# Kernel tuning notes

Hardware: AMD Instinct MI355X
Metric: run time of the kernel (lower is better)

The kernel has to match this reference:

```python
import jax, jax.numpy as jnp
import numpy as np

D_MODEL = 1024
N_HEADS = 16
D_HEAD = D_MODEL // N_HEADS
ROPE_BASE = 10000.0
EPS = float(jnp.finfo(jnp.float32).eps)  # torch RMSNorm default eps


def _rmsnorm(x, g):
    # x: (..., d_head), g: (d_head,)
    var = jnp.mean(x * x, axis=-1, keepdims=True)
    return x * jax.lax.rsqrt(var + EPS) * g


def _rope(x, pos):
    # x: (B, H, L, d), pos: (L,) int
    d = x.shape[-1]
    inv_freq = 1.0 / (ROPE_BASE ** (jnp.arange(0, d, 2, dtype=jnp.float32) / d))  # (d/2,)
    ang = pos.astype(jnp.float32)[:, None] * inv_freq[None, :]                    # (L, d/2)
    cos, sin = jnp.cos(ang), jnp.sin(ang)                                         # (L, d/2)
    x1, x2 = jnp.split(x, 2, axis=-1)
    return jnp.concatenate([x1 * cos - x2 * sin, x1 * sin + x2 * cos], axis=-1)


def setup_inputs() -> dict:
    key = jax.random.key(0)
    ks = jax.random.split(key, 6)
    B, Lq, Lk = 4, 2048, 2048
    s = 0.02
    return {
        "queries": jax.random.normal(ks[0], (B, Lq, D_MODEL), dtype=jnp.float32),
        "kv": jax.random.normal(ks[1], (B, Lk, D_MODEL), dtype=jnp.float32),
        "Wq": jax.random.normal(ks[2], (D_MODEL, D_MODEL), dtype=jnp.float32) * s,
        "Wkv": jax.random.normal(ks[3], (D_MODEL, 2 * D_MODEL), dtype=jnp.float32) * s,
        "Wout": jax.random.normal(ks[4], (D_MODEL, D_MODEL), dtype=jnp.float32) * s,
        "g_q": jnp.ones((D_HEAD,), dtype=jnp.float32),
        "g_k": jnp.ones((D_HEAD,), dtype=jnp.float32),
        "pos_q": jnp.arange(Lq, dtype=jnp.int64 if jax.config.jax_enable_x64 else jnp.int32),
        "pos_k": jnp.arange(Lk, dtype=jnp.int64 if jax.config.jax_enable_x64 else jnp.int32),
    }


def reference(queries, kv, Wq, Wkv, Wout, g_q, g_k, pos_q, pos_k):
    B, Lq, D = queries.shape
    Lk = kv.shape[1]
    H, d = N_HEADS, D_HEAD
    # projections (bias=False)
    q = (queries @ Wq).reshape(B, Lq, H, d).transpose(0, 2, 1, 3)          # (B,H,Lq,d)
    kvp = (kv @ Wkv).reshape(B, Lk, H, 2 * d).transpose(0, 2, 1, 3)        # (B,H,Lk,2d)
    k, v = kvp[..., :d], kvp[..., d:]
    # per-head RMSNorm on q/k
    q = _rmsnorm(q, g_q)
    k = _rmsnorm(k, g_k)
    # RoPE
    q = _rope(q, pos_q)
    k = _rope(k, pos_k)
    # attention (non-causal, no mask, no dropout)
    scale = d ** -0.5
    scores = jnp.einsum("bhqd,bhkd->bhqk", q, k) * scale                   # (B,H,Lq,Lk)
    attn = jax.nn.softmax(scores, axis=-1)
    y = jnp.einsum("bhqk,bhkd->bhqd", attn, v)                             # (B,H,Lq,d)
    y = y.transpose(0, 2, 1, 3).reshape(B, Lq, D)
    return y @ Wout
```

## Files before the change

kernel.cpp:

```cpp
#include <hip/hip_runtime.h>

#define DEVI __device__ __forceinline__

typedef __bf16 bf16;
typedef __attribute__((ext_vector_type(8))) __bf16 bf16x8v;
typedef __attribute__((ext_vector_type(4))) __bf16 bf16x4v;
typedef __attribute__((ext_vector_type(16))) float f32x16;

constexpr int LKV = 2048;

DEVI void gload16(const void* g, void* l) {
  __builtin_amdgcn_global_load_lds((__attribute__((address_space(1))) void*)g,
                                   (__attribute__((address_space(3))) void*)l, 16, 0, 0);
}

DEVI bf16x8v ldfrag(const bf16* base, int row, int clog) {
  int cphys = clog ^ (row & 7);
  return *(const bf16x8v*)(base + row * 64 + cphys * 8);
}

DEVI unsigned pk2(float a, float b) {
  unsigned short ha = __builtin_bit_cast(unsigned short, (__bf16)a);
  unsigned short hb = __builtin_bit_cast(unsigned short, (__bf16)b);
  return (unsigned)ha | ((unsigned)hb << 16);
}

__global__ void cast_bf16_kernel(const float* __restrict__ in, bf16* __restrict__ out, int n8) {
  int i = blockIdx.x * blockDim.x + threadIdx.x;
  if (i >= n8) return;
  long base = (long)i * 8;
  float4 a = *(const float4*)(in + base);
  float4 b = *(const float4*)(in + base + 4);
  bf16x8v v;
  v[0] = (bf16)a.x; v[1] = (bf16)a.y; v[2] = (bf16)a.z; v[3] = (bf16)a.w;
  v[4] = (bf16)b.x; v[5] = (bf16)b.y; v[6] = (bf16)b.z; v[7] = (bf16)b.w;
  *(bf16x8v*)(out + base) = v;
}

__global__ void wtrans_kernel(const float* __restrict__ W, bf16* __restrict__ Wt, int K, int N) {
  __shared__ float t[32][33];
  int n0 = blockIdx.x * 32, k0 = blockIdx.y * 32;
  int tx = threadIdx.x, ty = threadIdx.y;
  #pragma unroll
  for (int i = 0; i < 4; ++i) t[ty + i * 8][tx] = W[(long)(k0 + ty + i * 8) * N + n0 + tx];
  __syncthreads();
  #pragma unroll
  for (int i = 0; i < 4; ++i) Wt[(long)(n0 + ty + i * 8) * K + k0 + tx] = (bf16)t[tx][ty + i * 8];
}

template<bool OUT_BF16>
__global__ __launch_bounds__(256, 2)
void gemm_bf16_kernel(const bf16* __restrict__ A, const bf16* __restrict__ Bt,
                      void* __restrict__ C, int M, int N, int K, int NXB) {
  __shared__ bf16 As[128 * 64];
  __shared__ bf16 Bs[128 * 64];
  const int tid = threadIdx.x;
  const int wid = tid >> 6, lane = tid & 63;
  const int ln31 = lane & 31, hi = lane >> 5;
  const int wr = wid >> 1, wc = wid & 1;
  const int cpx = gridDim.x >> 3;
  const int wg = blockIdx.x;
  const int flat = (wg & 7) * cpx + (wg >> 3);
  const int by = flat / NXB, bx = flat - by * NXB;
  const int tM = by * 128, tN = bx * 128;
  f32x16 acc[2][2] = {};
  for (int kt = 0; kt < K; kt += 64) {
    #pragma unroll
    for (int p = 0; p < 8; ++p) {
      int cidx = p * 4 + wid;
      int row = (cidx & 15) * 8 + (lane >> 3);
      int clog = (lane & 7) ^ (row & 7);
      if (cidx < 16)
        gload16(A + (long)(tM + row) * K + kt + clog * 8, As + cidx * 512);
      else
        gload16(Bt + (long)(tN + row) * K + kt + clog * 8, Bs + (cidx - 16) * 512);
    }
    __syncthreads();
    #pragma unroll
    for (int st = 0; st < 4; ++st) {
      int clog = st * 2 + hi;
      bf16x8v a0 = ldfrag(As, wr * 64 + ln31, clog);
      bf16x8v a1 = ldfrag(As, wr * 64 + 32 + ln31, clog);
      bf16x8v b0 = ldfrag(Bs, wc * 64 + ln31, clog);
      bf16x8v b1 = ldfrag(Bs, wc * 64 + 32 + ln31, clog);
      acc[0][0] = __builtin_amdgcn_mfma_f32_32x32x16_bf16(a0, b0, acc[0][0], 0, 0, 0);
      acc[0][1] = __builtin_amdgcn_mfma_f32_32x32x16_bf16(a0, b1, acc[0][1], 0, 0, 0);
      acc[1][0] = __builtin_amdgcn_mfma_f32_32x32x16_bf16(a1, b0, acc[1][0], 0, 0, 0);
      acc[1][1] = __builtin_amdgcn_mfma_f32_32x32x16_bf16(a1, b1, acc[1][1], 0, 0, 0);
    }
    __syncthreads();
  }
  #pragma unroll
  for (int mi = 0; mi < 2; ++mi)
    #pragma unroll
    for (int ni = 0; ni < 2; ++ni)
      #pragma unroll
      for (int rr = 0; rr < 4; ++rr)
        #pragma unroll
        for (int j = 0; j < 4; ++j) {
          int mrow = tM + wr * 64 + mi * 32 + rr * 8 + hi * 4 + j;
          int ncol = tN + wc * 64 + ni * 32 + ln31;
          float v = acc[mi][ni][rr * 4 + j];
          if (OUT_BF16) ((bf16*)C)[(long)mrow * N + ncol] = (bf16)v;
          else          ((float*)C)[(long)mrow * N + ncol] = v;
        }
}

__global__ void rope_tab_kernel(const int* __restrict__ pos, float2* __restrict__ tab, float scale) {
  int idx = blockIdx.x * 256 + threadIdx.x;
  int l = idx >> 5, i = idx & 31;
  float ang = (float)pos[l] * __expf((float)i * -0.28782313662425575f);
  float sn, cs;
  sincosf(ang, &sn, &cs);
  tab[idx] = make_float2(cs * scale, sn * scale);
}

__global__ void rope_qk_kernel(const bf16* __restrict__ X, bf16* __restrict__ Out,
                               const float* __restrict__ g, const float2* __restrict__ tab,
                               int colStride, int colOff) {
  int tid = threadIdx.x; int wid = tid >> 6; int lane = tid & 63;
  long w = (long)blockIdx.x * 4 + wid;
  int h = (int)(w & 15); long bl = w >> 4;
  int l = (int)(bl & 2047); int b = (int)(bl >> 11);
  float x = (float)X[bl * colStride + h * colOff + lane];
  float ss = x * x;
  #pragma unroll
  for (int m = 32; m >= 1; m >>= 1) ss += __shfl_xor(ss, m);
  float rs = rsqrtf(ss * (1.0f / 64.0f) + 1.1920928955078125e-07f);
  x *= rs * g[lane];
  float other = __shfl_xor(x, 32);
  float2 cssn = tab[l * 32 + (lane & 31)];
  float y = x * cssn.x + ((lane < 32) ? -other : other) * cssn.y;
  int bh = b * 16 + h;
  Out[((long)bh * 2048 + l) * 64 + lane] = (bf16)y;
}

__global__ void transpose_v_kernel(const unsigned short* __restrict__ KVp, unsigned short* __restrict__ Vt) {
  __shared__ unsigned short t[64][65];
  int bh = blockIdx.y; int b = bh >> 4, h = bh & 15;
  long lt = (long)blockIdx.x * 64;
  int tid = threadIdx.x; int c = tid & 63; int r0 = tid >> 6;
  #pragma unroll
  for (int i = 0; i < 16; ++i) {
    int l = i * 4 + r0;
    t[l][c] = KVp[((long)(b * 2048) + lt + l) * 2048 + h * 128 + 64 + c];
  }
  __syncthreads();
  #pragma unroll
  for (int i = 0; i < 16; ++i) {
    int dv = i * 4 + r0;
    Vt[((long)(bh * 64 + dv)) * 2048 + lt + c] = t[c][dv];
  }
}

__global__ __launch_bounds__(256, 2)
void attn_kernel(const bf16* __restrict__ Q, const bf16* __restrict__ Kr,
                 const bf16* __restrict__ Vt, bf16* __restrict__ Y) {
  __shared__ bf16 Ks[2 * 4096];
  __shared__ bf16 Vs[2 * 4096];
  const int tid = threadIdx.x, wid = tid >> 6, lane = tid & 63;
  const int ln31 = lane & 31, hi = lane >> 5;
  const int wg = blockIdx.x;
  const int flat = (wg & 7) * 128 + (wg >> 3);
  const int bh = flat >> 4, qb = flat & 15;
  const int qg = qb * 128 + wid * 32 + ln31;

  const int rsub = lane >> 3, csub = lane & 7;
  int r0 = wid * 8 + rsub;        int s0 = csub ^ (r0 & 7);
  int r1 = (wid + 4) * 8 + rsub;  int s1 = csub ^ (r1 & 7);
  const bf16* gp0 = Kr + ((long)bh * 2048 + r0) * 64 + s0 * 8;
  const bf16* gp1 = Kr + ((long)bh * 2048 + r1) * 64 + s1 * 8;
  const bf16* gp2 = Vt + ((long)(bh * 64 + r0)) * 2048 + s0 * 8;
  const bf16* gp3 = Vt + ((long)(bh * 64 + r1)) * 2048 + s1 * 8;
  bf16* lk0 = Ks + wid * 512;
  bf16* lk1 = Ks + (wid + 4) * 512;
  bf16* lv0 = Vs + wid * 512;
  bf16* lv1 = Vs + (wid + 4) * 512;

  const bf16* Qrow = Q + ((long)bh * 2048 + qg) * 64;
  bf16x8v qf[4];
  #pragma unroll
  for (int st = 0; st < 4; ++st) qf[st] = *(const bf16x8v*)(Qrow + st * 16 + hi * 8);
  f32x16 o[2] = {};
  float srun = 0.0f;

  gload16(gp0, lk0); gp0 += 4096;
  gload16(gp1, lk1); gp1 += 4096;
  gload16(gp2, lv0); gp2 += 64;
  gload16(gp3, lv1); gp3 += 64;
  __syncthreads();

  int boff = 0;
  for (int kt = 0; kt < LKV; kt += 64) {
    if (kt + 64 < LKV) {
      int nb = boff ^ 4096;
      gload16(gp0, lk0 + nb); gp0 += 4096;
      gload16(gp1, lk1 + nb); gp1 += 4096;
      gload16(gp2, lv0 + nb); gp2 += 64;
      gload16(gp3, lv1 + nb); gp3 += 64;
    }
    const bf16* kb = Ks + boff;
    const bf16* vb = Vs + boff;

    f32x16 sT[2] = {};
    #pragma unroll
    for (int st = 0; st < 4; ++st) {
      int clog = st * 2 + hi;
      bf16x8v k0 = ldfrag(kb, ln31, clog);
      bf16x8v k1 = ldfrag(kb, 32 + ln31, clog);
      sT[0] = __builtin_amdgcn_mfma_f32_32x32x16_bf16(k0, qf[st], sT[0], 0, 0, 0);
      sT[1] = __builtin_amdgcn_mfma_f32_32x32x16_bf16(k1, qf[st], sT[1], 0, 0, 0);
    }

    float p0 = 0.0f, p1 = 0.0f, p2 = 0.0f, p3 = 0.0f;
    #pragma unroll
    for (int mf = 0; mf < 2; ++mf) {
      #pragma unroll
      for (int r = 0; r < 16; r += 4) {
        float e0 = __builtin_amdgcn_exp2f(sT[mf][r + 0]);
        float e1 = __builtin_amdgcn_exp2f(sT[mf][r + 1]);
        float e2 = __builtin_amdgcn_exp2f(sT[mf][r + 2]);
        float e3 = __builtin_amdgcn_exp2f(sT[mf][r + 3]);
        sT[mf][r + 0] = e0; sT[mf][r + 1] = e1; sT[mf][r + 2] = e2; sT[mf][r + 3] = e3;
        p0 += e0; p1 += e1; p2 += e2; p3 += e3;
      }
    }
    srun += (p0 + p1) + (p2 + p3);

    #pragma unroll
    for (int kb_ = 0; kb_ < 4; ++kb_) {
      int mf = kb_ >> 1; int rb = (kb_ & 1) * 8;
      unsigned w0 = pk2(sT[mf][rb + 0], sT[mf][rb + 1]);
      unsigned w1 = pk2(sT[mf][rb + 2], sT[mf][rb + 3]);
      unsigned w2 = pk2(sT[mf][rb + 4], sT[mf][rb + 5]);
      unsigned w3 = pk2(sT[mf][rb + 6], sT[mf][rb + 7]);
      asm("v_permlane32_swap_b32 %0, %1" : "+v"(w0), "+v"(w2));
      asm("v_permlane32_swap_b32 %0, %1" : "+v"(w1), "+v"(w3));
      uint4 uw = make_uint4(w0, w1, w2, w3);
      bf16x8v pf = __builtin_bit_cast(bf16x8v, uw);
      int clog = kb_ * 2 + hi;
      bf16x8v v0 = ldfrag(vb, ln31, clog);
      bf16x8v v1 = ldfrag(vb, 32 + ln31, clog);
      o[0] = __builtin_amdgcn_mfma_f32_32x32x16_bf16(v0, pf, o[0], 0, 0, 0);
      o[1] = __builtin_amdgcn_mfma_f32_32x32x16_bf16(v1, pf, o[1], 0, 0, 0);
    }
    __syncthreads();
    boff ^= 4096;
  }

  srun += __shfl_xor(srun, 32);
  float inv = 1.0f / srun;
  int b = bh >> 4, h = bh & 15;
  long orow = ((long)(b * 2048 + qg)) * 1024 + h * 64;
  #pragma unroll
  for (int mfo = 0; mfo < 2; ++mfo)
    #pragma unroll
    for (int rr = 0; rr < 4; ++rr) {
      bf16x4v wv;
      #pragma unroll
      for (int j = 0; j < 4; ++j) wv[j] = (bf16)(o[mfo][rr * 4 + j] * inv);
      *(bf16x4v*)(Y + orow + mfo * 32 + rr * 8 + hi * 4) = wv;
    }
}

extern "C" void kernel_launch(void* const* d_in, const int* in_sizes, int n_in,
                              void* d_out, int out_size, void* d_ws, size_t ws_size,
                              hipStream_t stream) {
  const float* queries = (const float*)d_in[0];
  const float* kv      = (const float*)d_in[1];
  const float* Wq      = (const float*)d_in[2];
  const float* Wkv     = (const float*)d_in[3];
  const float* Wout    = (const float*)d_in[4];
  const float* g_q     = (const float*)d_in[5];
  const float* g_k     = (const float*)d_in[6];
  const int*   pos_q   = (const int*)d_in[7];
  const int*   pos_k   = (const int*)d_in[8];

  char* ws = (char*)d_ws;
  bf16* Qb    = (bf16*)ws; ws += (long)8192 * 1024 * 2;
  bf16* KVb   = (bf16*)ws; ws += (long)8192 * 1024 * 2;
  bf16* Wqt   = (bf16*)ws; ws += (long)1024 * 1024 * 2;
  bf16* Wkvt  = (bf16*)ws; ws += (long)2048 * 1024 * 2;
  bf16* Woutt = (bf16*)ws; ws += (long)1024 * 1024 * 2;
  bf16* Qp    = (bf16*)ws; ws += (long)8192 * 1024 * 2;
  bf16* KVp   = (bf16*)ws; ws += (long)8192 * 2048 * 2;
  bf16* Qr    = (bf16*)ws; ws += (long)8192 * 1024 * 2;
  bf16* Kr    = (bf16*)ws; ws += (long)8192 * 1024 * 2;
  bf16* Vt    = (bf16*)ws; ws += (long)8192 * 1024 * 2;
  bf16* Y     = (bf16*)ws; ws += (long)8192 * 1024 * 2;
  float2* tabq = (float2*)ws; ws += (long)65536 * 8;
  float2* tabk = (float2*)ws; ws += (long)65536 * 8;

  rope_tab_kernel<<<256, 256, 0, stream>>>(pos_q, tabq, 0.18033688011112042f);
  rope_tab_kernel<<<256, 256, 0, stream>>>(pos_k, tabk, 1.0f);

  cast_bf16_kernel<<<4096, 256, 0, stream>>>(queries, Qb, 8192 * 1024 / 8);
  cast_bf16_kernel<<<4096, 256, 0, stream>>>(kv, KVb, 8192 * 1024 / 8);
  wtrans_kernel<<<dim3(32, 32), dim3(32, 8), 0, stream>>>(Wq, Wqt, 1024, 1024);
  wtrans_kernel<<<dim3(64, 32), dim3(32, 8), 0, stream>>>(Wkv, Wkvt, 1024, 2048);
  wtrans_kernel<<<dim3(32, 32), dim3(32, 8), 0, stream>>>(Wout, Woutt, 1024, 1024);

  gemm_bf16_kernel<true><<<512, 256, 0, stream>>>(Qb, Wqt, Qp, 8192, 1024, 1024, 8);
  gemm_bf16_kernel<true><<<1024, 256, 0, stream>>>(KVb, Wkvt, KVp, 8192, 2048, 1024, 16);

  rope_qk_kernel<<<32768, 256, 0, stream>>>(Qp, Qr, g_q, tabq, 1024, 64);
  rope_qk_kernel<<<32768, 256, 0, stream>>>(KVp, Kr, g_k, tabk, 2048, 128);
  transpose_v_kernel<<<dim3(32, 64), 256, 0, stream>>>((const unsigned short*)KVp, (unsigned short*)Vt);

  attn_kernel<<<1024, 256, 0, stream>>>(Qr, Kr, Vt, Y);

  gemm_bf16_kernel<false><<<512, 256, 0, stream>>>(Y, Woutt, d_out, 8192, 1024, 1024, 8);
}
```

Baseline: 367.2 us.

## Add 256x256-tile multi-stage GEMM for KV projection and raise MFMA priority

```diff
diff --git a/kernel.cpp b/kernel.cpp
--- a/kernel.cpp
+++ b/kernel.cpp
@@ -106,6 +106,85 @@
         }
 }
 
+DEVI void stage_region(const bf16* __restrict__ A, const bf16* __restrict__ Bt,
+                       long tM, long tN, int K, int s, bf16* Lds, int tid) {
+  bf16* region = Lds + ((((s >> 1) & 1) << 1) | (s & 1)) * 16384;
+  int kcol = (s >> 1) * 64 + (s & 1) * 32;
+  #pragma unroll
+  for (int q = 0; q < 4; ++q) {
+    int ci = q * 512 + tid;
+    int row = ci >> 3, phys = ci & 7;
+    int clog = phys ^ (row & 7);
+    const bf16* src = (clog < 4)
+      ? A  + (tM + row) * K + kcol + clog * 8
+      : Bt + (tN + row) * K + kcol + (clog - 4) * 8;
+    gload16(src, region + ci * 8);
+  }
+}
+
+__global__ __launch_bounds__(512, 2)
+void gemm256_kernel(const bf16* __restrict__ A, const bf16* __restrict__ Bt,
+                    bf16* __restrict__ C, int M, int N, int K, int NXB) {
+  __shared__ bf16 Lds[4 * 16384];
+  const int tid = threadIdx.x;
+  const int wid = tid >> 6, lane = tid & 63;
+  const int ln31 = lane & 31, hi = lane >> 5;
+  const int wm = wid >> 2, wn = wid & 3;
+  const int cpx = gridDim.x >> 3;
+  const int wg = blockIdx.x;
+  const int flat = (wg & 7) * cpx + (wg >> 3);
+  const int by = flat / NXB, bx = flat - by * NXB;
+  const long tM = (long)by * 256, tN = (long)bx * 256;
+  const int NS = (K >> 6) * 2;
+
+  f32x16 acc[4][2] = {};
+
+  stage_region(A, Bt, tM, tN, K, 0, Lds, tid);
+  stage_region(A, Bt, tM, tN, K, 1, Lds, tid);
+  stage_region(A, Bt, tM, tN, K, 2, Lds, tid);
+
+  for (int s = 0; s < NS; ++s) {
+    asm volatile("s_waitcnt vmcnt(8)" ::: "memory");
+    __builtin_amdgcn_s_barrier();
+    __builtin_amdgcn_sched_barrier(0);
+    stage_region(A, Bt, tM, tN, K, s + 3, Lds, tid);
+    const bf16* R = Lds + ((((s >> 1) & 1) << 1) | (s & 1)) * 16384;
+    bf16x8v a[4][2], b[2][2];
+    #pragma unroll
+    for (int mi = 0; mi < 4; ++mi)
+      #pragma unroll
+      for (int ks = 0; ks < 2; ++ks)
+        a[mi][ks] = ldfrag(R, wm * 128 + mi * 32 + ln31, ks * 2 + hi);
+    #pragma unroll
+    for (int ni = 0; ni < 2; ++ni)
+      #pragma unroll
+      for (int ks = 0; ks < 2; ++ks)
+        b[ni][ks] = ldfrag(R, wn * 64 + ni * 32 + ln31, 4 + ks * 2 + hi);
+    __builtin_amdgcn_s_setprio(1);
+    #pragma unroll
+    for (int ks = 0; ks < 2; ++ks)
+      #pragma unroll
+      for (int mi = 0; mi < 4; ++mi)
+        #pragma unroll
+        for (int ni = 0; ni < 2; ++ni)
+          acc[mi][ni] = __builtin_amdgcn_mfma_f32_32x32x16_bf16(a[mi][ks], b[ni][ks], acc[mi][ni], 0, 0, 0);
+    __builtin_amdgcn_s_setprio(0);
+  }
+
+  #pragma unroll
+  for (int mi = 0; mi < 4; ++mi)
+    #pragma unroll
+    for (int ni = 0; ni < 2; ++ni)
+      #pragma unroll
+      for (int rr = 0; rr < 4; ++rr)
+        #pragma unroll
+        for (int j = 0; j < 4; ++j) {
+          long mrow = tM + wm * 128 + mi * 32 + rr * 8 + hi * 4 + j;
+          long ncol = tN + wn * 64 + ni * 32 + ln31;
+          C[mrow * N + ncol] = (bf16)acc[mi][ni][rr * 4 + j];
+        }
+}
+
 __global__ void rope_tab_kernel(const int* __restrict__ pos, float2* __restrict__ tab, float scale) {
   int idx = blockIdx.x * 256 + threadIdx.x;
   int l = idx >> 5, i = idx & 31;
@@ -203,6 +282,7 @@
     const bf16* vb = Vs + boff;
 
     f32x16 sT[2] = {};
+    __builtin_amdgcn_s_setprio(1);
     #pragma unroll
     for (int st = 0; st < 4; ++st) {
       int clog = st * 2 + hi;
@@ -211,6 +291,7 @@
       sT[0] = __builtin_amdgcn_mfma_f32_32x32x16_bf16(k0, qf[st], sT[0], 0, 0, 0);
       sT[1] = __builtin_amdgcn_mfma_f32_32x32x16_bf16(k1, qf[st], sT[1], 0, 0, 0);
     }
+    __builtin_amdgcn_s_setprio(0);
 
     float p0 = 0.0f, p1 = 0.0f, p2 = 0.0f, p3 = 0.0f;
     #pragma unroll
@@ -227,6 +308,7 @@
     }
     srun += (p0 + p1) + (p2 + p3);
 
+    __builtin_amdgcn_s_setprio(1);
     #pragma unroll
     for (int kb_ = 0; kb_ < 4; ++kb_) {
       int mf = kb_ >> 1; int rb = (kb_ & 1) * 8;
@@ -244,6 +326,7 @@
       o[0] = __builtin_amdgcn_mfma_f32_32x32x16_bf16(v0, pf, o[0], 0, 0, 0);
       o[1] = __builtin_amdgcn_mfma_f32_32x32x16_bf16(v1, pf, o[1], 0, 0, 0);
     }
+    __builtin_amdgcn_s_setprio(0);
     __syncthreads();
     boff ^= 4096;
   }
@@ -301,7 +384,7 @@
   wtrans_kernel<<<dim3(32, 32), dim3(32, 8), 0, stream>>>(Wout, Woutt, 1024, 1024);
 
   gemm_bf16_kernel<true><<<512, 256, 0, stream>>>(Qb, Wqt, Qp, 8192, 1024, 1024, 8);
-  gemm_bf16_kernel<true><<<1024, 256, 0, stream>>>(KVb, Wkvt, KVp, 8192, 2048, 1024, 16);
+  gemm256_kernel<<<256, 512, 0, stream>>>(KVb, Wkvt, KVp, 8192, 2048, 1024, 8);
 
   rope_qk_kernel<<<32768, 256, 0, stream>>>(Qp, Qr, g_q, tabq, 1024, 64);
   rope_qk_kernel<<<32768, 256, 0, stream>>>(KVp, Kr, g_k, tabk, 2048, 128);
```

New measurement: 357.8 us. -2.6%, faster.
